# Kernel tuning notes

Hardware: AMD Instinct MI355X
Metric: run time of the kernel (lower is better)

The kernel has to match this reference:

```python
import jax, jax.numpy as jnp
import numpy as np

B, N, C, HF, WF, D = 2, 6, 64, 112, 200, 64
BEV_H, BEV_W = 200, 200


def _view_matrix(h, w, h_m=100.0, w_m=100.0, offset=0.0):
    sh, sw = h / h_m, w / w_m
    return np.array([[0.0, -sw, w / 2.0],
                     [-sh, 0.0, h * offset + h / 2.0],
                     [0.0, 0.0, 1.0]], dtype=np.float32)


def setup_inputs() -> dict:
    key = jax.random.key(0)
    k1, k2 = jax.random.split(key)
    feat_bn = jax.random.normal(k1, (B * N, C, HF, WF), jnp.float32)
    depth_prob = jax.nn.softmax(jax.random.normal(k2, (B * N, D, HF, WF), jnp.float32), axis=1)
    # structured inverse intrinsics (pinhole, f = W/2)
    f = 0.5 * WF
    K = np.array([[f, 0.0, WF / 2.0], [0.0, f, HF / 2.0], [0.0, 0.0, 1.0]], np.float32)
    I_inv = np.broadcast_to(np.linalg.inv(K).astype(np.float32), (B, N, 3, 3)).copy()
    # random rigid cam->ego extrinsics inverse: orthonormal rotation + translation, cam height 1.5m
    rng = np.random.default_rng(0)
    E_inv = np.tile(np.eye(4, dtype=np.float32), (B, N, 1, 1))
    for bi in range(B):
        for ni in range(N):
            Q, _ = np.linalg.qr(rng.normal(size=(3, 3)))
            E_inv[bi, ni, :3, :3] = Q.astype(np.float32)
            E_inv[bi, ni, :3, 3] = np.array([rng.uniform(-2, 2), rng.uniform(-2, 2), 1.5], np.float32)
    V = jnp.asarray(_view_matrix(BEV_H, BEV_W))
    feat_hw = jnp.array([HF, WF], jnp.int32)
    return {"feat_bn": feat_bn, "depth_prob": depth_prob, "I_inv": jnp.asarray(I_inv),
            "E_inv": jnp.asarray(E_inv), "V": V, "feat_hw": feat_hw, "n": N}


def reference(feat_bn, depth_prob, I_inv, E_inv, V, feat_hw, n):
    bn, Cc, h, w = feat_bn.shape
    b = bn // n
    hw = h * w
    HW = BEV_H * BEV_W
    dt = feat_bn.dtype

    # pixel grid; source does rearrange('d w h -> d (h w)') on an [3,h,w] tensor,
    # i.e. flattens with the *width* axis outer -> transpose before reshape (bug-faithful).
    u, v = jnp.meshgrid(jnp.arange(w, dtype=dt), jnp.arange(h, dtype=dt))  # each [h, w]
    pix = jnp.stack([u, v, jnp.ones_like(u)], 0)          # [3, h, w]
    pix = pix.transpose(0, 2, 1).reshape(3, hw)           # [3, hw]

    I_inv_bn = I_inv.reshape(bn, 3, 3)
    E_inv_bn = E_inv.reshape(bn, 4, 4)
    cam = jnp.einsum('bij,jp->bip', I_inv_bn, pix)        # [bn, 3, hw]
    cam = jnp.concatenate([cam, jnp.ones((bn, 1, hw), dt)], axis=1)  # pad homogeneous 1
    d = jnp.einsum('bij,bjp->bip', E_inv_bn, cam).transpose(0, 2, 1)[..., :3]  # [bn, hw, 3]
    c = E_inv_bn[:, :3, 3][:, None, :]                    # [bn, 1, 3] camera center

    # ray-ground intersection (z = 0 plane)
    s = -c[..., 2] / jnp.maximum(d[..., 2], 1e-6)
    xy_ego = c[..., :2] + d[..., :2] * s[..., None]       # [bn, hw, 2]

    # ego -> BEV pixel coords via view matrix V
    homo = jnp.concatenate([xy_ego, jnp.ones_like(xy_ego[..., :1])], axis=-1)
    proj = homo @ V.T
    bev_xy = proj[..., :2] / jnp.maximum(proj[..., 2:], 1e-7)

    gx = bev_xy[..., 0] / (BEV_W - 1) * 2 - 1
    gy = bev_xy[..., 1] / (BEV_H - 1) * 2 - 1
    conf = depth_prob.max(axis=1).reshape(bn, hw)          # [bn, hw]

    px = (gx + 1) * (BEV_W - 1) / 2
    py = (gy + 1) * (BEV_H - 1) / 2
    x0 = jnp.clip(jnp.floor(px), 0, BEV_W - 1)
    y0 = jnp.clip(jnp.floor(py), 0, BEV_H - 1)
    x1 = jnp.clip(x0 + 1, 0, BEV_W - 1)
    y1 = jnp.clip(y0 + 1, 0, BEV_H - 1)

    corners = [(x0, y0, (x1 - px) * (y1 - py)),
               (x1, y0, (px - x0) * (y1 - py)),
               (x0, y1, (x1 - px) * (py - y0)),
               (x1, y1, (px - x0) * (py - y0))]

    idx = jnp.concatenate([y.astype(jnp.int32) * BEV_W + x.astype(jnp.int32)
                           for x, y, _ in corners], axis=1)             # [bn, 4hw]
    wgt = jnp.concatenate([wg * conf for _, _, wg in corners], axis=1)  # [bn, 4hw]

    feat_flat = feat_bn.reshape(bn, Cc, hw)
    wfeat = jnp.tile(feat_flat, (1, 1, 4)) * wgt[:, None, :]            # [bn, C, 4hw]

    idx_flat = (idx + jnp.arange(bn, dtype=jnp.int32)[:, None] * HW).reshape(-1)
    vals = wfeat.transpose(0, 2, 1).reshape(-1, Cc)                      # [bn*4hw, C]
    bev = jax.ops.segment_sum(vals, idx_flat, num_segments=bn * HW)      # [bn*HW, C]
    bev = bev.reshape(b, n, HW, Cc).transpose(0, 1, 3, 2).reshape(b, n, Cc, BEV_H, BEV_W)
    return bev.mean(axis=1)
```

## Files before the change

kernel.cpp:

```cpp
#include <hip/hip_runtime.h>

#define BB   2
#define NN   6
#define CCH  64
#define HFE  112
#define WFE  200
#define DDE  64
#define HWF  (HFE*WFE)
#define HWF4 (HWF/4)
#define BEVH 200
#define BEVW 200
#define HWB  (BEVH*BEVW)
#define NBINS (BB*HWB)
#define NBINS_PAD 81920
#define NSCANB (NBINS_PAD/256)
#define MAXENT1 (BB*NN*HWF)
#define NCHUNK1 (MAXENT1/64)
#define ACC_ELEMS ((size_t)BB*HWB*CCH)

__device__ __forceinline__ float4 f4max(float4 a, float4 b) {
    return make_float4(fmaxf(a.x,b.x), fmaxf(a.y,b.y), fmaxf(a.z,b.z), fmaxf(a.w,b.w));
}

struct Geo {
    int valid;
    int c00, c10, c01, c11;
    float w00, w10, w01, w11;
};

__device__ __forceinline__ Geo geo_compute(int bn, int p,
    const float* __restrict__ I_inv, const float* __restrict__ E_inv,
    const float* __restrict__ Vm)
{
    Geo g; g.valid = 0;
    const float u = (float)(p / HFE);
    const float v = (float)(p % HFE);
    const float* Ii = I_inv + bn * 9;
    const float* Ei = E_inv + bn * 16;
    float cx = Ii[0]*u + Ii[1]*v + Ii[2];
    float cy = Ii[3]*u + Ii[4]*v + Ii[5];
    float cz = Ii[6]*u + Ii[7]*v + Ii[8];
    float tx = Ei[3], ty = Ei[7], tz = Ei[11];
    float dx = Ei[0]*cx + Ei[1]*cy + Ei[2] *cz + tx;
    float dy = Ei[4]*cx + Ei[5]*cy + Ei[6] *cz + ty;
    float dz = Ei[8]*cx + Ei[9]*cy + Ei[10]*cz + tz;
    float s  = -tz / fmaxf(dz, 1e-6f);
    float ex = tx + dx * s;
    float ey = ty + dy * s;
    float prx = Vm[0]*ex + Vm[1]*ey + Vm[2];
    float pry = Vm[3]*ex + Vm[4]*ey + Vm[5];
    float prz = Vm[6]*ex + Vm[7]*ey + Vm[8];
    float den = fmaxf(prz, 1e-7f);
    float bx = prx / den, by = pry / den;
    float gx = bx / (float)(BEVW-1) * 2.0f - 1.0f;
    float gy = by / (float)(BEVH-1) * 2.0f - 1.0f;
    float px = (gx + 1.0f) * (float)(BEVW-1) / 2.0f;
    float py = (gy + 1.0f) * (float)(BEVH-1) / 2.0f;
    float x0f = fminf(fmaxf(floorf(px), 0.0f), (float)(BEVW-1));
    float y0f = fminf(fmaxf(floorf(py), 0.0f), (float)(BEVH-1));
    float x1f = fminf(x0f + 1.0f, (float)(BEVW-1));
    float y1f = fminf(y0f + 1.0f, (float)(BEVH-1));
    if (x0f == x1f || y0f == y1f) return g;
    float wx0 = x1f - px, wx1 = px - x0f;
    float wy0 = y1f - py, wy1 = py - y0f;
    int x0 = (int)x0f, x1 = (int)x1f, y0 = (int)y0f, y1 = (int)y1f;
    g.c00 = y0*BEVW + x0;  g.w00 = wx0*wy0;
    g.c10 = y0*BEVW + x1;  g.w10 = wx1*wy0;
    g.c01 = y1*BEVW + x0;  g.w01 = wx0*wy1;
    g.c11 = y1*BEVW + x1;  g.w11 = wx1*wy1;
    g.valid = 1;
    return g;
}

__device__ __forceinline__ void run_info(int cell, int lane,
                                         bool& leader, int& runlen, int& leadlane)
{
    int prev = __shfl_up(cell, 1);
    bool change = (lane == 0) || (cell != prev);
    unsigned long long bal = __ballot(change);
    unsigned long long below = bal & (~0ull >> (63 - lane));
    leadlane = 63 - __builtin_clzll(below);
    unsigned long long above = (lane == 63) ? 0ull : (bal >> (lane + 1));
    int next = (above == 0ull) ? 64 : (lane + 1 + __builtin_ffsll((long long)above) - 1);
    runlen = next - lane;
    leader = change && (cell >= 0);
}

__device__ __forceinline__ unsigned pack2w(float a, float b) {
    unsigned ua = __float2uint_rn(a * 65535.0f);
    unsigned ub = __float2uint_rn(b * 65535.0f);
    return ua | (ub << 16);
}

__global__ __launch_bounds__(256) void prep_kernel(
    const float* __restrict__ feat,
    const float* __restrict__ depth,
    const float* __restrict__ I_inv, const float* __restrict__ E_inv,
    const float* __restrict__ Vm,
    float* __restrict__ feat_t,
    float* __restrict__ conf,
    int* __restrict__ counts)
{
    __shared__ float tile[4][16][68];

    const int bn   = blockIdx.y;
    const int p0   = blockIdx.x * 64;
    const int tid  = threadIdx.x;
    const int lane = tid & 63, wv = tid >> 6;
    const int lq   = lane & 3;
    const int lh   = lane >> 2;
    const int pw   = p0 + 16 * wv;

    const float* fcam = feat + (size_t)bn * CCH * HWF;
    float4 f[4];
#pragma unroll
    for (int i = 0; i < 4; ++i)
        f[i] = *(const float4*)(fcam + (size_t)(16*i + lh) * HWF + pw + 4*lq);

    const float* dcam = depth + (size_t)bn * DDE * HWF;
    float4 mx;
    {
        float4 d0 = *(const float4*)(dcam + (size_t)(lh     ) * HWF + pw + 4*lq);
        float4 d1 = *(const float4*)(dcam + (size_t)(lh + 16) * HWF + pw + 4*lq);
        float4 d2 = *(const float4*)(dcam + (size_t)(lh + 32) * HWF + pw + 4*lq);
        float4 d3 = *(const float4*)(dcam + (size_t)(lh + 48) * HWF + pw + 4*lq);
        mx = f4max(f4max(d0, d1), f4max(d2, d3));
    }

#pragma unroll
    for (int i = 0; i < 4; ++i) {
        tile[wv][4*lq + 0][16*i + lh] = f[i].x;
        tile[wv][4*lq + 1][16*i + lh] = f[i].y;
        tile[wv][4*lq + 2][16*i + lh] = f[i].z;
        tile[wv][4*lq + 3][16*i + lh] = f[i].w;
    }

#pragma unroll
    for (int m = 4; m <= 32; m <<= 1) {
        mx.x = fmaxf(mx.x, __shfl_xor(mx.x, m));
        mx.y = fmaxf(mx.y, __shfl_xor(mx.y, m));
        mx.z = fmaxf(mx.z, __shfl_xor(mx.z, m));
        mx.w = fmaxf(mx.w, __shfl_xor(mx.w, m));
    }
    if (lh == 0)
        *(float4*)(conf + (size_t)bn * HWF + pw + 4*lq) = mx;

    float* ocam = feat_t + (size_t)bn * HWF * CCH;
#pragma unroll
    for (int r = 0; r < 4; ++r) {
        float4 o = *(const float4*)(&tile[wv][lh][16*r + 4*lq]);
        *(float4*)(ocam + (size_t)(pw + lh) * CCH + 16*r + 4*lq) = o;
    }

    if (wv == 0) {
        Geo g = geo_compute(bn, p0 + lane, I_inv, E_inv, Vm);
        const int base = (bn / NN) * HWB;
        const int cell = g.valid ? base + g.c00 : -1;
        bool leader; int runlen, leadlane;
        run_info(cell, lane, leader, runlen, leadlane);
        if (leader) atomicAdd(&counts[cell], runlen);
    }
}

__global__ __launch_bounds__(256) void scan1_kernel(
    const int* __restrict__ counts, int* __restrict__ offsets, int* __restrict__ bsum)
{
    __shared__ int tmp[256];
    const int t = threadIdx.x;
    const int i = blockIdx.x * 256 + t;
    int v = counts[i];
    tmp[t] = v; __syncthreads();
    for (int off = 1; off < 256; off <<= 1) {
        int x = (t >= off) ? tmp[t - off] : 0;
        __syncthreads();
        tmp[t] += x;
        __syncthreads();
    }
    offsets[i] = tmp[t] - v;
    if (t == 255) bsum[blockIdx.x] = tmp[255];
}

__global__ __launch_bounds__(256) void scan3_kernel(
    int* __restrict__ offsets, const int* __restrict__ bsum, int* __restrict__ cursor)
{
    __shared__ int s[256];
    const int t = threadIdx.x;
    int part = 0;
    for (int i = t; i < blockIdx.x; i += 256) part += bsum[i];
    s[t] = part; __syncthreads();
    for (int off = 128; off > 0; off >>= 1) {
        if (t < off) s[t] += s[t + off];
        __syncthreads();
    }
    const int i = blockIdx.x * 256 + t;
    int v = offsets[i] + s[0];
    offsets[i] = v;
    cursor[i]  = v;
}

__global__ __launch_bounds__(256) void place_kernel(
    const float* __restrict__ conf,
    const float* __restrict__ I_inv, const float* __restrict__ E_inv,
    const float* __restrict__ Vm,
    int* __restrict__ cursor, uint4* __restrict__ entries)
{
    const int bn = blockIdx.y;
    const int p  = blockIdx.x * blockDim.x + threadIdx.x;
    const int lane = threadIdx.x & 63;
    const int inb = (p < HWF);
    const int pp = inb ? p : HWF - 1;
    Geo g = geo_compute(bn, pp, I_inv, E_inv, Vm);
    const int valid = inb && g.valid;
    if (__ballot(valid) == 0ull) return;
    const int base = (bn / NN) * HWB;
    const int bin  = valid ? base + g.c00 : -1;

    bool leader; int runlen, leadlane;
    run_info(bin, lane, leader, runlen, leadlane);
    int pos_leader = 0;
    if (leader) pos_leader = atomicAdd(&cursor[bin], runlen);
    int pos = __shfl(pos_leader, leadlane) + (lane - leadlane);
    if (valid) {
        const float cf = conf[(size_t)bn * HWF + pp];
        entries[pos] = make_uint4((unsigned)bin, (unsigned)(bn * HWF + pp),
                                  pack2w(g.w00 * cf, g.w10 * cf),
                                  pack2w(g.w01 * cf, g.w11 * cf));
    }
}

__global__ __launch_bounds__(256) void gather_seg_kernel(
    const uint4* __restrict__ entries, const int* __restrict__ total_ptr,
    const float* __restrict__ feat_t, float* __restrict__ acc)
{
    const int lane = threadIdx.x & 63, wv = threadIdx.x >> 6;
    const int chunk = blockIdx.x * 4 + wv;
    const int total = *total_ptr;
    const int start = chunk * 64;
    if (start >= total) return;
    const int m = min(64, total - start);

    int myb = -1;
    uint4 mye = make_uint4(0u, 0u, 0u, 0u);
    if (lane < m) { mye = entries[start + lane]; myb = (int)mye.x; }

    const float inv = 1.0f / 65535.0f;
    float a00 = 0.f, a10 = 0.f, a01 = 0.f, a11 = 0.f;
    for (int j = 0; j < 64; j += 8) {
        int bb[9]; unsigned px[8], wA[8], wB[8];
#pragma unroll
        for (int k = 0; k < 8; ++k) {
            bb[k] = __shfl(myb, j + k);
            px[k] = (unsigned)__shfl((int)mye.y, j + k);
            wA[k] = (unsigned)__shfl((int)mye.z, j + k);
            wB[k] = (unsigned)__shfl((int)mye.w, j + k);
        }
        bb[8] = (j + 8 < 64) ? __shfl(myb, j + 8) : -2;
        float f[8];
#pragma unroll
        for (int k = 0; k < 8; ++k)
            f[k] = (bb[k] >= 0) ? feat_t[(size_t)px[k] * CCH + lane] : 0.0f;
#pragma unroll
        for (int k = 0; k < 8; ++k) {
            a00 = fmaf(f[k], (float)(wA[k] & 0xffffu) * inv, a00);
            a10 = fmaf(f[k], (float)(wA[k] >> 16)     * inv, a10);
            a01 = fmaf(f[k], (float)(wB[k] & 0xffffu) * inv, a01);
            a11 = fmaf(f[k], (float)(wB[k] >> 16)     * inv, a11);
            if (bb[k] != bb[k + 1]) {
                if (bb[k] >= 0) {
                    float* ab = acc + (size_t)bb[k] * CCH + lane;
                    atomicAdd(ab,                       a00);
                    atomicAdd(ab + (size_t)1   * CCH,   a10);
                    atomicAdd(ab + (size_t)200 * CCH,   a01);
                    atomicAdd(ab + (size_t)201 * CCH,   a11);
                }
                a00 = a10 = a01 = a11 = 0.f;
            }
        }
    }
}

__global__ __launch_bounds__(256) void finalize_kernel(
    const float* __restrict__ acc, float* __restrict__ out)
{
    __shared__ float t[64][66];
    const int b     = blockIdx.y;
    const int cell0 = blockIdx.x * 64;
    const int cc    = threadIdx.x >> 2;
    const int q     = threadIdx.x & 3;

    const float* abase = acc + ((size_t)b * HWB + cell0) * CCH;
#pragma unroll
    for (int i = 0; i < 4; ++i) {
        const int cg = q + 4 * i;
        float4 f = *(const float4*)(abase + (size_t)cc * CCH + 4 * cg);
        t[cc][4*cg+0] = f.x; t[cc][4*cg+1] = f.y;
        t[cc][4*cg+2] = f.z; t[cc][4*cg+3] = f.w;
    }
    __syncthreads();
    float* obase = out + (size_t)b * CCH * HWB + cell0;
#pragma unroll
    for (int i = 0; i < 4; ++i) {
        const int lg = q + 4 * i;
        float4 o;
        o.x = t[4*lg+0][cc] * (1.0f/6.0f);
        o.y = t[4*lg+1][cc] * (1.0f/6.0f);
        o.z = t[4*lg+2][cc] * (1.0f/6.0f);
        o.w = t[4*lg+3][cc] * (1.0f/6.0f);
        *(float4*)(obase + (size_t)cc * HWB + 4 * lg) = o;
    }
}

__global__ __launch_bounds__(256) void splat_kernel(
    const float* __restrict__ feat, const float* __restrict__ depth,
    const float* __restrict__ I_inv, const float* __restrict__ E_inv,
    const float* __restrict__ Vm, float* __restrict__ acc)
{
    __shared__ float fshare[64][65];
    __shared__ float cpart2[4][64];
    const int bn = blockIdx.y, b = bn / NN, p0 = blockIdx.x * 64;
    const int lane = threadIdx.x & 63, wv = threadIdx.x >> 6;
    const float* fbase = feat + (size_t)bn * CCH * HWF + p0;
#pragma unroll
    for (int c = wv; c < CCH; c += 4)
        fshare[lane][c] = fbase[(size_t)c * HWF + lane];
    const float* dbase = depth + (size_t)bn * DDE * HWF + p0;
    float m = dbase[(size_t)(wv * 16) * HWF + lane];
#pragma unroll
    for (int d = wv * 16 + 1; d < wv * 16 + 16; ++d)
        m = fmaxf(m, dbase[(size_t)d * HWF + lane]);
    cpart2[wv][lane] = m;
    __syncthreads();
    float* ab = acc + ((size_t)b * HWB) * CCH + lane;
    for (int s = wv * 16; s < wv * 16 + 16; ++s) {
        Geo g = geo_compute(bn, p0 + s, I_inv, E_inv, Vm);
        if (!g.valid) continue;
        float cf = fmaxf(fmaxf(cpart2[0][s], cpart2[1][s]), fmaxf(cpart2[2][s], cpart2[3][s]));
        float f = fshare[s][lane];
        atomicAdd(ab + (size_t)g.c00 * CCH, f * (g.w00 * cf));
        atomicAdd(ab + (size_t)g.c10 * CCH, f * (g.w10 * cf));
        atomicAdd(ab + (size_t)g.c01 * CCH, f * (g.w01 * cf));
        atomicAdd(ab + (size_t)g.c11 * CCH, f * (g.w11 * cf));
    }
}

extern "C" void kernel_launch(void* const* d_in, const int* in_sizes, int n_in,
                              void* d_out, int out_size, void* d_ws, size_t ws_size,
                              hipStream_t stream) {
    const float* feat  = (const float*)d_in[0];
    const float* depth = (const float*)d_in[1];
    const float* I_inv = (const float*)d_in[2];
    const float* E_inv = (const float*)d_in[3];
    const float* Vm    = (const float*)d_in[4];
    float* out = (float*)d_out;

    size_t off = 0;
    char* wsb = (char*)d_ws;
    auto carve = [&](size_t bytes) -> void* {
        void* p = wsb + off; off += (bytes + 255) & ~(size_t)255; return p;
    };
    float* feat_t  = (float*)carve((size_t)BB * NN * CCH * HWF * 4);
    float* acc     = (float*)carve(ACC_ELEMS * 4);
    int*   counts  = (int*)  carve((NBINS_PAD + 256) * 4);
    uint4* entries = (uint4*)carve((size_t)MAXENT1 * 16);
    float* conf    = (float*)carve((size_t)BB * NN * HWF * 4);
    int*   offsets = (int*)  carve((NBINS_PAD + 256) * 4);
    int*   cursor  = (int*)  carve((NBINS_PAD + 256) * 4);
    int*   bsum    = (int*)  carve(NSCANB * 4);

    if (off <= ws_size) {
        hipMemsetAsync(acc, 0, ACC_ELEMS * 4 + (NBINS_PAD + 256) * 4, stream);

        dim3 pgrid(HWF / 64, BB * NN);
        prep_kernel<<<pgrid, 256, 0, stream>>>(feat, depth, I_inv, E_inv, Vm,
                                               feat_t, conf, counts);

        scan1_kernel<<<NSCANB, 256, 0, stream>>>(counts, offsets, bsum);
        scan3_kernel<<<NSCANB, 256, 0, stream>>>(offsets, bsum, cursor);

        dim3 plgrid((HWF + 255) / 256, BB * NN);
        place_kernel<<<plgrid, 256, 0, stream>>>(conf, I_inv, E_inv, Vm,
                                                 cursor, entries);

        gather_seg_kernel<<<NCHUNK1 / 4, 256, 0, stream>>>(
            entries, offsets + NBINS, feat_t, acc);

        dim3 fgrid(HWB / 64, BB);
        finalize_kernel<<<fgrid, 256, 0, stream>>>(acc, out);
    } else {
        float* acc0 = (float*)d_ws;
        hipMemsetAsync(acc0, 0, ACC_ELEMS * 4, stream);
        dim3 grid(HWF / 64, BB * NN);
        splat_kernel<<<grid, 256, 0, stream>>>(feat, depth, I_inv, E_inv, Vm, acc0);
        dim3 fgrid(HWB / 64, BB);
        finalize_kernel<<<fgrid, 256, 0, stream>>>(acc0, out);
    }
}
```

Baseline: 247.3 us.

## Replace sort-by-bin pipeline with fused splat kernel using run-merged atomics

Drops the multi-kernel counting-sort pipeline (prep, two scan passes, place, gather) along with the transposed feature and entries buffers. A single fused kernel loads features and depth max into shared memory and computes geometry once per pixel. Each wave then walks its 16 pixels and accumulates consecutive pixels that land in the same BEV bin before issuing the four atomics. This removes several launches and the large intermediate traffic. In exchange, atomic contention on the BEV accumulator may rise, because merging only happens within short local runs instead of across a globally sorted list.

Result: slower. 299.9 us (+21.3%).

```diff
diff --git a/kernel.cpp b/kernel.cpp
--- a/kernel.cpp
+++ b/kernel.cpp
@@ -7,24 +7,14 @@
 #define WFE  200
 #define DDE  64
 #define HWF  (HFE*WFE)
-#define HWF4 (HWF/4)
 #define BEVH 200
 #define BEVW 200
 #define HWB  (BEVH*BEVW)
-#define NBINS (BB*HWB)
-#define NBINS_PAD 81920
-#define NSCANB (NBINS_PAD/256)
-#define MAXENT1 (BB*NN*HWF)
-#define NCHUNK1 (MAXENT1/64)
 #define ACC_ELEMS ((size_t)BB*HWB*CCH)
-
-__device__ __forceinline__ float4 f4max(float4 a, float4 b) {
-    return make_float4(fmaxf(a.x,b.x), fmaxf(a.y,b.y), fmaxf(a.z,b.z), fmaxf(a.w,b.w));
-}
 
 struct Geo {
     int valid;
-    int c00, c10, c01, c11;
+    int c00;
     float w00, w10, w01, w11;
 };
 
@@ -32,7 +22,8 @@
     const float* __restrict__ I_inv, const float* __restrict__ E_inv,
     const float* __restrict__ Vm)
 {
-    Geo g; g.valid = 0;
+    Geo g; g.valid = 0; g.c00 = -1;
+    g.w00 = g.w10 = g.w01 = g.w11 = 0.f;
     const float u = (float)(p / HFE);
     const float v = (float)(p % HFE);
     const float* Ii = I_inv + bn * 9;
@@ -63,219 +54,85 @@
     if (x0f == x1f || y0f == y1f) return g;
     float wx0 = x1f - px, wx1 = px - x0f;
     float wy0 = y1f - py, wy1 = py - y0f;
-    int x0 = (int)x0f, x1 = (int)x1f, y0 = (int)y0f, y1 = (int)y1f;
-    g.c00 = y0*BEVW + x0;  g.w00 = wx0*wy0;
-    g.c10 = y0*BEVW + x1;  g.w10 = wx1*wy0;
-    g.c01 = y1*BEVW + x0;  g.w01 = wx0*wy1;
-    g.c11 = y1*BEVW + x1;  g.w11 = wx1*wy1;
+    int x0 = (int)x0f, y0 = (int)y0f;
+    g.c00 = y0*BEVW + x0;
+    g.w00 = wx0*wy0;  g.w10 = wx1*wy0;
+    g.w01 = wx0*wy1;  g.w11 = wx1*wy1;
     g.valid = 1;
     return g;
 }
 
-__device__ __forceinline__ void run_info(int cell, int lane,
-                                         bool& leader, int& runlen, int& leadlane)
-{
-    int prev = __shfl_up(cell, 1);
-    bool change = (lane == 0) || (cell != prev);
-    unsigned long long bal = __ballot(change);
-    unsigned long long below = bal & (~0ull >> (63 - lane));
-    leadlane = 63 - __builtin_clzll(below);
-    unsigned long long above = (lane == 63) ? 0ull : (bal >> (lane + 1));
-    int next = (above == 0ull) ? 64 : (lane + 1 + __builtin_ffsll((long long)above) - 1);
-    runlen = next - lane;
-    leader = change && (cell >= 0);
-}
-
-__device__ __forceinline__ unsigned pack2w(float a, float b) {
-    unsigned ua = __float2uint_rn(a * 65535.0f);
-    unsigned ub = __float2uint_rn(b * 65535.0f);
-    return ua | (ub << 16);
-}
-
-__global__ __launch_bounds__(256) void prep_kernel(
+__global__ __launch_bounds__(256) void fused_splat_kernel(
     const float* __restrict__ feat,
     const float* __restrict__ depth,
     const float* __restrict__ I_inv, const float* __restrict__ E_inv,
     const float* __restrict__ Vm,
-    float* __restrict__ feat_t,
-    float* __restrict__ conf,
-    int* __restrict__ counts)
+    float* __restrict__ acc)
 {
-    __shared__ float tile[4][16][68];
+    __shared__ float fshare[64][65];
+    __shared__ float cpart[4][64];
+    __shared__ int   gbin[64];
+    __shared__ float gwgt[64][4];
 
-    const int bn   = blockIdx.y;
-    const int p0   = blockIdx.x * 64;
-    const int tid  = threadIdx.x;
+    const int bn  = blockIdx.y;
+    const int p0  = blockIdx.x * 64;
+    const int tid = threadIdx.x;
     const int lane = tid & 63, wv = tid >> 6;
-    const int lq   = lane & 3;
-    const int lh   = lane >> 2;
-    const int pw   = p0 + 16 * wv;
 
-    const float* fcam = feat + (size_t)bn * CCH * HWF;
-    float4 f[4];
+    const float* fbase = feat + (size_t)bn * CCH * HWF + p0;
 #pragma unroll
-    for (int i = 0; i < 4; ++i)
-        f[i] = *(const float4*)(fcam + (size_t)(16*i + lh) * HWF + pw + 4*lq);
+    for (int c = wv; c < CCH; c += 4)
+        fshare[lane][c] = fbase[(size_t)c * HWF + lane];
 
-    const float* dcam = depth + (size_t)bn * DDE * HWF;
-    float4 mx;
-    {
-        float4 d0 = *(const float4*)(dcam + (size_t)(lh     ) * HWF + pw + 4*lq);
-        float4 d1 = *(const float4*)(dcam + (size_t)(lh + 16) * HWF + pw + 4*lq);
-        float4 d2 = *(const float4*)(dcam + (size_t)(lh + 32) * HWF + pw + 4*lq);
-        float4 d3 = *(const float4*)(dcam + (size_t)(lh + 48) * HWF + pw + 4*lq);
-        mx = f4max(f4max(d0, d1), f4max(d2, d3));
+    const float* dbase = depth + (size_t)bn * DDE * HWF + p0;
+    float m = dbase[(size_t)(wv * 16) * HWF + lane];
+#pragma unroll
+    for (int d = 1; d < 16; ++d)
+        m = fmaxf(m, dbase[(size_t)(wv * 16 + d) * HWF + lane]);
+    cpart[wv][lane] = m;
+
+    if (tid < 64) {
+        Geo g = geo_compute(bn, p0 + tid, I_inv, E_inv, Vm);
+        const int base = (bn / NN) * HWB;
+        gbin[tid] = g.valid ? base + g.c00 : -1;
+        gwgt[tid][0] = g.w00; gwgt[tid][1] = g.w10;
+        gwgt[tid][2] = g.w01; gwgt[tid][3] = g.w11;
     }
+    __syncthreads();
 
+    float a00 = 0.f, a10 = 0.f, a01 = 0.f, a11 = 0.f;
+    int prev = -1;
 #pragma unroll
-    for (int i = 0; i < 4; ++i) {
-        tile[wv][4*lq + 0][16*i + lh] = f[i].x;
-        tile[wv][4*lq + 1][16*i + lh] = f[i].y;
-        tile[wv][4*lq + 2][16*i + lh] = f[i].z;
-        tile[wv][4*lq + 3][16*i + lh] = f[i].w;
-    }
-
-#pragma unroll
-    for (int m = 4; m <= 32; m <<= 1) {
-        mx.x = fmaxf(mx.x, __shfl_xor(mx.x, m));
-        mx.y = fmaxf(mx.y, __shfl_xor(mx.y, m));
-        mx.z = fmaxf(mx.z, __shfl_xor(mx.z, m));
-        mx.w = fmaxf(mx.w, __shfl_xor(mx.w, m));
-    }
-    if (lh == 0)
-        *(float4*)(conf + (size_t)bn * HWF + pw + 4*lq) = mx;
-
-    float* ocam = feat_t + (size_t)bn * HWF * CCH;
-#pragma unroll
-    for (int r = 0; r < 4; ++r) {
-        float4 o = *(const float4*)(&tile[wv][lh][16*r + 4*lq]);
-        *(float4*)(ocam + (size_t)(pw + lh) * CCH + 16*r + 4*lq) = o;
-    }
-
-    if (wv == 0) {
-        Geo g = geo_compute(bn, p0 + lane, I_inv, E_inv, Vm);
-        const int base = (bn / NN) * HWB;
-        const int cell = g.valid ? base + g.c00 : -1;
-        bool leader; int runlen, leadlane;
-        run_info(cell, lane, leader, runlen, leadlane);
-        if (leader) atomicAdd(&counts[cell], runlen);
-    }
-}
-
-__global__ __launch_bounds__(256) void scan1_kernel(
-    const int* __restrict__ counts, int* __restrict__ offsets, int* __restrict__ bsum)
-{
-    __shared__ int tmp[256];
-    const int t = threadIdx.x;
-    const int i = blockIdx.x * 256 + t;
-    int v = counts[i];
-    tmp[t] = v; __syncthreads();
-    for (int off = 1; off < 256; off <<= 1) {
-        int x = (t >= off) ? tmp[t - off] : 0;
-        __syncthreads();
-        tmp[t] += x;
-        __syncthreads();
-    }
-    offsets[i] = tmp[t] - v;
-    if (t == 255) bsum[blockIdx.x] = tmp[255];
-}
-
-__global__ __launch_bounds__(256) void scan3_kernel(
-    int* __restrict__ offsets, const int* __restrict__ bsum, int* __restrict__ cursor)
-{
-    __shared__ int s[256];
-    const int t = threadIdx.x;
-    int part = 0;
-    for (int i = t; i < blockIdx.x; i += 256) part += bsum[i];
-    s[t] = part; __syncthreads();
-    for (int off = 128; off > 0; off >>= 1) {
-        if (t < off) s[t] += s[t + off];
-        __syncthreads();
-    }
-    const int i = blockIdx.x * 256 + t;
-    int v = offsets[i] + s[0];
-    offsets[i] = v;
-    cursor[i]  = v;
-}
-
-__global__ __launch_bounds__(256) void place_kernel(
-    const float* __restrict__ conf,
-    const float* __restrict__ I_inv, const float* __restrict__ E_inv,
-    const float* __restrict__ Vm,
-    int* __restrict__ cursor, uint4* __restrict__ entries)
-{
-    const int bn = blockIdx.y;
-    const int p  = blockIdx.x * blockDim.x + threadIdx.x;
-    const int lane = threadIdx.x & 63;
-    const int inb = (p < HWF);
-    const int pp = inb ? p : HWF - 1;
-    Geo g = geo_compute(bn, pp, I_inv, E_inv, Vm);
-    const int valid = inb && g.valid;
-    if (__ballot(valid) == 0ull) return;
-    const int base = (bn / NN) * HWB;
-    const int bin  = valid ? base + g.c00 : -1;
-
-    bool leader; int runlen, leadlane;
-    run_info(bin, lane, leader, runlen, leadlane);
-    int pos_leader = 0;
-    if (leader) pos_leader = atomicAdd(&cursor[bin], runlen);
-    int pos = __shfl(pos_leader, leadlane) + (lane - leadlane);
-    if (valid) {
-        const float cf = conf[(size_t)bn * HWF + pp];
-        entries[pos] = make_uint4((unsigned)bin, (unsigned)(bn * HWF + pp),
-                                  pack2w(g.w00 * cf, g.w10 * cf),
-                                  pack2w(g.w01 * cf, g.w11 * cf));
-    }
-}
-
-__global__ __launch_bounds__(256) void gather_seg_kernel(
-    const uint4* __restrict__ entries, const int* __restrict__ total_ptr,
-    const float* __restrict__ feat_t, float* __restrict__ acc)
-{
-    const int lane = threadIdx.x & 63, wv = threadIdx.x >> 6;
-    const int chunk = blockIdx.x * 4 + wv;
-    const int total = *total_ptr;
-    const int start = chunk * 64;
-    if (start >= total) return;
-    const int m = min(64, total - start);
-
-    int myb = -1;
-    uint4 mye = make_uint4(0u, 0u, 0u, 0u);
-    if (lane < m) { mye = entries[start + lane]; myb = (int)mye.x; }
-
-    const float inv = 1.0f / 65535.0f;
-    float a00 = 0.f, a10 = 0.f, a01 = 0.f, a11 = 0.f;
-    for (int j = 0; j < 64; j += 8) {
-        int bb[9]; unsigned px[8], wA[8], wB[8];
-#pragma unroll
-        for (int k = 0; k < 8; ++k) {
-            bb[k] = __shfl(myb, j + k);
-            px[k] = (unsigned)__shfl((int)mye.y, j + k);
-            wA[k] = (unsigned)__shfl((int)mye.z, j + k);
-            wB[k] = (unsigned)__shfl((int)mye.w, j + k);
-        }
-        bb[8] = (j + 8 < 64) ? __shfl(myb, j + 8) : -2;
-        float f[8];
-#pragma unroll
-        for (int k = 0; k < 8; ++k)
-            f[k] = (bb[k] >= 0) ? feat_t[(size_t)px[k] * CCH + lane] : 0.0f;
-#pragma unroll
-        for (int k = 0; k < 8; ++k) {
-            a00 = fmaf(f[k], (float)(wA[k] & 0xffffu) * inv, a00);
-            a10 = fmaf(f[k], (float)(wA[k] >> 16)     * inv, a10);
-            a01 = fmaf(f[k], (float)(wB[k] & 0xffffu) * inv, a01);
-            a11 = fmaf(f[k], (float)(wB[k] >> 16)     * inv, a11);
-            if (bb[k] != bb[k + 1]) {
-                if (bb[k] >= 0) {
-                    float* ab = acc + (size_t)bb[k] * CCH + lane;
-                    atomicAdd(ab,                       a00);
-                    atomicAdd(ab + (size_t)1   * CCH,   a10);
-                    atomicAdd(ab + (size_t)200 * CCH,   a01);
-                    atomicAdd(ab + (size_t)201 * CCH,   a11);
-                }
+    for (int i = 0; i < 16; ++i) {
+        const int s   = wv * 16 + i;
+        const int bin = gbin[s];
+        if (bin != prev) {
+            if (prev >= 0) {
+                float* ab = acc + (size_t)prev * CCH + lane;
+                atomicAdd(ab,                     a00);
+                atomicAdd(ab + (size_t)1   * CCH, a10);
+                atomicAdd(ab + (size_t)200 * CCH, a01);
+                atomicAdd(ab + (size_t)201 * CCH, a11);
                 a00 = a10 = a01 = a11 = 0.f;
             }
+            prev = bin;
         }
+        if (bin >= 0) {
+            const float cf = fmaxf(fmaxf(cpart[0][s], cpart[1][s]),
+                                   fmaxf(cpart[2][s], cpart[3][s]));
+            const float f = fshare[s][lane];
+            a00 = fmaf(f, gwgt[s][0] * cf, a00);
+            a10 = fmaf(f, gwgt[s][1] * cf, a10);
+            a01 = fmaf(f, gwgt[s][2] * cf, a01);
+            a11 = fmaf(f, gwgt[s][3] * cf, a11);
+        }
+    }
+    if (prev >= 0) {
+        float* ab = acc + (size_t)prev * CCH + lane;
+        atomicAdd(ab,                     a00);
+        atomicAdd(ab + (size_t)1   * CCH, a10);
+        atomicAdd(ab + (size_t)200 * CCH, a01);
+        atomicAdd(ab + (size_t)201 * CCH, a11);
     }
 }
 
@@ -310,39 +167,6 @@
     }
 }
 
-__global__ __launch_bounds__(256) void splat_kernel(
-    const float* __restrict__ feat, const float* __restrict__ depth,
-    const float* __restrict__ I_inv, const float* __restrict__ E_inv,
-    const float* __restrict__ Vm, float* __restrict__ acc)
-{
-    __shared__ float fshare[64][65];
-    __shared__ float cpart2[4][64];
-    const int bn = blockIdx.y, b = bn / NN, p0 = blockIdx.x * 64;
-    const int lane = threadIdx.x & 63, wv = threadIdx.x >> 6;
-    const float* fbase = feat + (size_t)bn * CCH * HWF + p0;
-#pragma unroll
-    for (int c = wv; c < CCH; c += 4)
-        fshare[lane][c] = fbase[(size_t)c * HWF + lane];
-    const float* dbase = depth + (size_t)bn * DDE * HWF + p0;
-    float m = dbase[(size_t)(wv * 16) * HWF + lane];
-#pragma unroll
-    for (int d = wv * 16 + 1; d < wv * 16 + 16; ++d)
-        m = fmaxf(m, dbase[(size_t)d * HWF + lane]);
-    cpart2[wv][lane] = m;
-    __syncthreads();
-    float* ab = acc + ((size_t)b * HWB) * CCH + lane;
-    for (int s = wv * 16; s < wv * 16 + 16; ++s) {
-        Geo g = geo_compute(bn, p0 + s, I_inv, E_inv, Vm);
-        if (!g.valid) continue;
-        float cf = fmaxf(fmaxf(cpart2[0][s], cpart2[1][s]), fmaxf(cpart2[2][s], cpart2[3][s]));
-        float f = fshare[s][lane];
-        atomicAdd(ab + (size_t)g.c00 * CCH, f * (g.w00 * cf));
-        atomicAdd(ab + (size_t)g.c10 * CCH, f * (g.w10 * cf));
-        atomicAdd(ab + (size_t)g.c01 * CCH, f * (g.w01 * cf));
-        atomicAdd(ab + (size_t)g.c11 * CCH, f * (g.w11 * cf));
-    }
-}
-
 extern "C" void kernel_launch(void* const* d_in, const int* in_sizes, int n_in,
                               void* d_out, int out_size, void* d_ws, size_t ws_size,
                               hipStream_t stream) {
@@ -353,45 +177,12 @@
     const float* Vm    = (const float*)d_in[4];
     float* out = (float*)d_out;
 
-    size_t off = 0;
-    char* wsb = (char*)d_ws;
-    auto carve = [&](size_t bytes) -> void* {
-        void* p = wsb + off; off += (bytes + 255) & ~(size_t)255; return p;
-    };
-    float* feat_t  = (float*)carve((size_t)BB * NN * CCH * HWF * 4);
-    float* acc     = (float*)carve(ACC_ELEMS * 4);
-    int*   counts  = (int*)  carve((NBINS_PAD + 256) * 4);
-    uint4* entries = (uint4*)carve((size_t)MAXENT1 * 16);
-    float* conf    = (float*)carve((size_t)BB * NN * HWF * 4);
-    int*   offsets = (int*)  carve((NBINS_PAD + 256) * 4);
-    int*   cursor  = (int*)  carve((NBINS_PAD + 256) * 4);
-    int*   bsum    = (int*)  carve(NSCANB * 4);
+    float* acc = (float*)d_ws;
+    hipMemsetAsync(acc, 0, ACC_ELEMS * 4, stream);
 
-    if (off <= ws_size) {
-        hipMemsetAsync(acc, 0, ACC_ELEMS * 4 + (NBINS_PAD + 256) * 4, stream);
+    dim3 sgrid(HWF / 64, BB * NN);
+    fused_splat_kernel<<<sgrid, 256, 0, stream>>>(feat, depth, I_inv, E_inv, Vm, acc);
 
-        dim3 pgrid(HWF / 64, BB * NN);
-        prep_kernel<<<pgrid, 256, 0, stream>>>(feat, depth, I_inv, E_inv, Vm,
-                                               feat_t, conf, counts);
-
-        scan1_kernel<<<NSCANB, 256, 0, stream>>>(counts, offsets, bsum);
-        scan3_kernel<<<NSCANB, 256, 0, stream>>>(offsets, bsum, cursor);
-
-        dim3 plgrid((HWF + 255) / 256, BB * NN);
-        place_kernel<<<plgrid, 256, 0, stream>>>(conf, I_inv, E_inv, Vm,
-                                                 cursor, entries);
-
-        gather_seg_kernel<<<NCHUNK1 / 4, 256, 0, stream>>>(
-            entries, offsets + NBINS, feat_t, acc);
-
-        dim3 fgrid(HWB / 64, BB);
-        finalize_kernel<<<fgrid, 256, 0, stream>>>(acc, out);
-    } else {
-        float* acc0 = (float*)d_ws;
-        hipMemsetAsync(acc0, 0, ACC_ELEMS * 4, stream);
-        dim3 grid(HWF / 64, BB * NN);
-        splat_kernel<<<grid, 256, 0, stream>>>(feat, depth, I_inv, E_inv, Vm, acc0);
-        dim3 fgrid(HWB / 64, BB);
-        finalize_kernel<<<fgrid, 256, 0, stream>>>(acc0, out);
-    }
+    dim3 fgrid(HWB / 64, BB);
+    finalize_kernel<<<fgrid, 256, 0, stream>>>(acc, out);
 }
```
